# Optimization experiments

Hardware: AMD Instinct MI355X
Metric: run time of the kernel (lower is better)

Reference implementation:

```python
import jax, jax.numpy as jnp
import numpy as np

# RT-DETR multi-scale deformable attention reference (PPMSDeformableAttention forward, value_mask=None)
SPATIAL_SHAPES = ((80, 80), (40, 40), (20, 20))  # (H, W) per level; sum(H*W) = 8400 = Len_v
NUM_HEADS = 8
NUM_LEVELS = 3
NUM_POINTS = 4


def _gather_corner(v_l, ix, iy, H, W):
    # v_l: [bs, heads, H*W, hd]; ix/iy: [bs, heads, N] int32 pixel indices (possibly out of range)
    valid = (ix >= 0) & (ix < W) & (iy >= 0) & (iy < H)
    idx = jnp.clip(iy, 0, H - 1) * W + jnp.clip(ix, 0, W - 1)
    g = jnp.take_along_axis(v_l, idx[..., None], axis=2)  # [bs, heads, N, hd]
    return jnp.where(valid[..., None], g, jnp.zeros((), v_l.dtype))


def _bilinear_sample(v_l, px, py, H, W):
    # grid_sample(align_corners=False, padding_mode='zeros') semantics.
    # v_l: [bs, heads, H*W, hd]; px/py: [bs, heads, N] continuous pixel coords
    x0 = jnp.floor(px).astype(jnp.int32)
    y0 = jnp.floor(py).astype(jnp.int32)
    x1, y1 = x0 + 1, y0 + 1
    wx1 = px - x0.astype(px.dtype)
    wy1 = py - y0.astype(py.dtype)
    wx0, wy0 = 1.0 - wx1, 1.0 - wy1
    out = (_gather_corner(v_l, x0, y0, H, W) * (wx0 * wy0)[..., None]
           + _gather_corner(v_l, x1, y0, H, W) * (wx1 * wy0)[..., None]
           + _gather_corner(v_l, x0, y1, H, W) * (wx0 * wy1)[..., None]
           + _gather_corner(v_l, x1, y1, H, W) * (wx1 * wy1)[..., None])
    return out  # [bs, heads, N, hd]


def setup_inputs() -> dict:
    key = jax.random.key(0)
    ks = jax.random.split(key, 8)
    bs, Lq, C = 32, 300, 256
    Lv = sum(h * w for h, w in SPATIAL_SHAPES)
    tp = NUM_HEADS * NUM_LEVELS * NUM_POINTS  # 96
    s = 1.0 / np.sqrt(C)
    return {
        "query": jax.random.normal(ks[0], (bs, Lq, C), jnp.float32),
        "reference_points": jax.random.uniform(ks[1], (bs, Lq, NUM_LEVELS, 4), jnp.float32, 0.05, 0.95),
        "value": jax.random.normal(ks[2], (bs, Lv, C), jnp.float32),
        "Wv": jax.random.normal(ks[3], (C, C), jnp.float32) * s,
        "bv": jnp.zeros((C,), jnp.float32),
        "Woff": jax.random.normal(ks[4], (C, tp * 2), jnp.float32) * (s * 0.1),
        "boff": jax.random.normal(ks[5], (tp * 2,), jnp.float32) * 0.5,
        "Watt": jax.random.normal(ks[6], (C, tp), jnp.float32) * s,
        "batt": jnp.zeros((tp,), jnp.float32),
        "Wout": jax.random.normal(ks[7], (C, C), jnp.float32) * s,
        "bout": jnp.zeros((C,), jnp.float32),
    }


def reference(query, reference_points, value, Wv, bv, Woff, boff, Watt, batt, Wout, bout):
    bs, Lq, C = query.shape
    H_, L, P = NUM_HEADS, NUM_LEVELS, NUM_POINTS
    hd = C // H_
    Lv = value.shape[1]

    # value projection -> [bs, heads, Lv, hd]
    v = (value @ Wv + bv).reshape(bs, Lv, H_, hd).transpose(0, 2, 1, 3)

    # sampling offsets and attention weights from query
    off = (query @ Woff + boff).reshape(bs, Lq, H_, L, P, 2)
    attw = jax.nn.softmax((query @ Watt + batt).reshape(bs, Lq, H_, L * P), axis=-1)
    attw = attw.reshape(bs, Lq, H_, L, P)

    # reference_points last dim == 4: (cx, cy, w, h) normalized
    ref_xy = reference_points[:, :, None, :, None, :2]  # [bs,Lq,1,L,1,2]
    ref_wh = reference_points[:, :, None, :, None, 2:]
    loc = ref_xy + off / P * ref_wh * 0.5  # [bs,Lq,H,L,P,2], normalized [0,1]

    out = jnp.zeros((bs, Lq, H_, hd), query.dtype)
    start = 0
    for l, (H, W) in enumerate(SPATIAL_SHAPES):
        v_l = v[:, :, start:start + H * W]  # [bs, heads, H*W, hd]
        start += H * W
        # normalized -> pixel coords (align_corners=False): p = loc * size - 0.5
        locl = loc[:, :, :, l]  # [bs, Lq, heads, P, 2]
        px = locl[..., 0] * W - 0.5
        py = locl[..., 1] * H - 0.5
        # [bs, Lq, heads, P] -> [bs, heads, Lq*P]
        px = px.transpose(0, 2, 1, 3).reshape(bs, H_, Lq * P)
        py = py.transpose(0, 2, 1, 3).reshape(bs, H_, Lq * P)
        sampled = _bilinear_sample(v_l, px, py, H, W)  # [bs, heads, Lq*P, hd]
        sampled = sampled.reshape(bs, H_, Lq, P, hd)
        out = out + jnp.einsum('bhqpd,bqhp->bqhd', sampled, attw[:, :, :, l])

    out = out.reshape(bs, Lq, C)
    return out @ Wout + bout
```

## Files before the change

kernel.cpp:

```cpp
#include <hip/hip_runtime.h>
#include <hip/hip_bf16.h>

#define BS 32
#define LQ 300
#define CDIM 256
#define HEADS 8
#define HD 32
#define NLEVELS 3
#define NPOINTS 4
#define LV 8400
#define NOA 288

typedef __attribute__((ext_vector_type(4))) float f32x4;
typedef __attribute__((ext_vector_type(8))) short short8;
typedef __attribute__((ext_vector_type(8))) unsigned short u16x8;
typedef __attribute__((ext_vector_type(4))) unsigned short u16x4;

__device__ __forceinline__ unsigned short f2bf(float f) {
    __hip_bfloat16 h = __float2bfloat16(f);
    return __bfloat16_as_ushort(h);
}
__device__ __forceinline__ float bf2f(unsigned short u) {
    union { unsigned u; float f; } v; v.u = ((unsigned)u) << 16;
    return v.f;
}

__global__ void prep_weights_kernel(
    const float* __restrict__ Wv, const float* __restrict__ Wout,
    const float* __restrict__ Woff, const float* __restrict__ Watt,
    unsigned short* __restrict__ WvT, unsigned short* __restrict__ WoutT,
    unsigned short* __restrict__ WoaT)
{
    const int bid = blockIdx.x;
    const int k = threadIdx.x;
    if (bid < 256) {
        WvT[bid * 256 + k] = f2bf(Wv[k * 256 + bid]);
    } else if (bid < 512) {
        const int n = bid - 256;
        WoutT[n * 256 + k] = f2bf(Wout[k * 256 + n]);
    } else {
        const int n = bid - 512;
        const float w = (n < 192) ? Woff[k * 192 + n] : Watt[k * 96 + (n - 192)];
        WoaT[n * 256 + k] = f2bf(w);
    }
}

#define BM 128
#define BK 32
#define PAD 40
#define EP2 136
#define NT (CDIM / BK)

__global__ __launch_bounds__(256) void proj_value_mfma(
    const float* __restrict__ value, const unsigned short* __restrict__ WvT,
    const float* __restrict__ bv, unsigned short* __restrict__ vout)
{
    __shared__ alignas(16) unsigned short lds_raw[17408];
    unsigned short* lds_x = lds_raw;
    unsigned short* lds_ep = lds_raw;

    const int tid = threadIdx.x;
    const int lane = tid & 63;
    const int wave = tid >> 6;
    const int la = lane & 15;
    const int lg = lane >> 4;

    const int orig = blockIdx.x;
    const int xcd = orig & 7, lin = orig >> 3;
    const int bid = xcd * 525 + lin;
    const int n0 = (bid & 1) * 128;
    const long row0 = (long)(bid >> 1) * BM;

    const int sr = tid >> 1;
    const int sk = (tid & 1) * 16;
    const float* xptr = value + (row0 + sr) * (long)CDIM + sk;

    const unsigned short* wlane = WvT + (size_t)(n0 + wave * 32 + la) * CDIM + lg * 8;

    f32x4 xrg[4];

    auto load_tile = [&](int kb) {
        const float* p = xptr + kb;
        xrg[0] = *(const f32x4*)(p);
        xrg[1] = *(const f32x4*)(p + 4);
        xrg[2] = *(const f32x4*)(p + 8);
        xrg[3] = *(const f32x4*)(p + 12);
    };
    auto write_tile = [&](int buf) {
        u16x8 t0, t1;
#pragma unroll
        for (int i = 0; i < 4; ++i) {
            t0[i]     = f2bf(xrg[0][i]);
            t0[i + 4] = f2bf(xrg[1][i]);
            t1[i]     = f2bf(xrg[2][i]);
            t1[i + 4] = f2bf(xrg[3][i]);
        }
        u16x8* wx = (u16x8*)&lds_x[buf * (128 * PAD) + sr * PAD + sk];
        wx[0] = t0; wx[1] = t1;
    };

    f32x4 acc[2][8] = {};

    load_tile(0);
    write_tile(0);
    __syncthreads();
    int cur = 0;

#pragma unroll
    for (int t = 0; t < NT; ++t) {
        if (t + 1 < NT) load_tile((t + 1) * BK);

        short8 wf[2];
#pragma unroll
        for (int nf = 0; nf < 2; ++nf)
            wf[nf] = *(const short8*)(wlane + (size_t)nf * 16 * CDIM + t * 32);

        const unsigned short* px = &lds_x[cur * (128 * PAD) + la * PAD + lg * 8];
#pragma unroll
        for (int mf = 0; mf < 8; ++mf) {
            const short8 xf = *(const short8*)(px + mf * 16 * PAD);
#pragma unroll
            for (int nf = 0; nf < 2; ++nf)
                acc[nf][mf] = __builtin_amdgcn_mfma_f32_16x16x32_bf16(
                    wf[nf], xf, acc[nf][mf], 0, 0, 0);
        }

        if (t + 1 < NT) write_tile(cur ^ 1);
        __syncthreads();
        cur ^= 1;
    }

#pragma unroll
    for (int nf = 0; nf < 2; ++nf) {
        const int nbl = wave * 32 + nf * 16 + lg * 4;
        const f32x4 bb = *(const f32x4*)&bv[n0 + nbl];
#pragma unroll
        for (int mf = 0; mf < 8; ++mf) {
            const int mloc = mf * 16 + la;
            u16x4 o;
#pragma unroll
            for (int j = 0; j < 4; ++j) o[j] = f2bf(acc[nf][mf][j] + bb[j]);
            *(u16x4*)&lds_ep[mloc * EP2 + nbl] = o;
        }
    }
    __syncthreads();
    {
        const int er = tid >> 1;
        const int ec = (tid & 1) * 64;
        const u16x8* src = (const u16x8*)&lds_ep[er * EP2 + ec];
        u16x8* dst = (u16x8*)&vout[(row0 + er) * CDIM + n0 + ec];
#pragma unroll
        for (int i = 0; i < 8; ++i) dst[i] = src[i];
    }
}

#define APAD 40
#define BPAD 40

__global__ __launch_bounds__(256) void offatt_gemm_mfma(
    const float* __restrict__ query, const unsigned short* __restrict__ WoaT,
    const float* __restrict__ boff, const float* __restrict__ batt,
    float* __restrict__ offatt)
{
    __shared__ unsigned short lds_a[2][BM * APAD];
    __shared__ unsigned short lds_b[2][NOA * BPAD];

    const int tid = threadIdx.x;
    const int lane = tid & 63;
    const int wave = tid >> 6;
    const int wm = wave >> 1;
    const int wn = wave & 1;
    const long row0 = (long)blockIdx.x * BM;

    const int ar = tid >> 1;
    const int ak = (tid & 1) * 16;
    const float* aptr = query + (row0 + ar) * CDIM + ak;
    const unsigned short* bptr  = WoaT + (size_t)tid * CDIM;
    const unsigned short* bptr2 = WoaT + (size_t)(256 + tid) * CDIM;
    const bool extra = tid < 32;

    f32x4 arg[4];
    u16x8 brg[4], brg2[4];

    auto load_tile = [&](int kb) {
        const float* p = aptr + kb;
        arg[0] = *(const f32x4*)(p);
        arg[1] = *(const f32x4*)(p + 4);
        arg[2] = *(const f32x4*)(p + 8);
        arg[3] = *(const f32x4*)(p + 12);
        const u16x8* q = (const u16x8*)(bptr + kb);
        brg[0] = q[0]; brg[1] = q[1]; brg[2] = q[2]; brg[3] = q[3];
        if (extra) {
            const u16x8* q2 = (const u16x8*)(bptr2 + kb);
            brg2[0] = q2[0]; brg2[1] = q2[1]; brg2[2] = q2[2]; brg2[3] = q2[3];
        }
    };
    auto write_tile = [&](int buf) {
        u16x8 t0, t1;
#pragma unroll
        for (int i = 0; i < 4; ++i) {
            t0[i]     = f2bf(arg[0][i]);
            t0[i + 4] = f2bf(arg[1][i]);
            t1[i]     = f2bf(arg[2][i]);
            t1[i + 4] = f2bf(arg[3][i]);
        }
        u16x8* wa = (u16x8*)&lds_a[buf][ar * APAD + ak];
        wa[0] = t0; wa[1] = t1;
        u16x8* wb = (u16x8*)&lds_b[buf][tid * BPAD];
        wb[0] = brg[0]; wb[1] = brg[1]; wb[2] = brg[2]; wb[3] = brg[3];
        if (extra) {
            u16x8* wb2 = (u16x8*)&lds_b[buf][(256 + tid) * BPAD];
            wb2[0] = brg2[0]; wb2[1] = brg2[1]; wb2[2] = brg2[2]; wb2[3] = brg2[3];
        }
    };

    f32x4 acc[4][9] = {};
    const int la = lane & 15;
    const int lg = lane >> 4;

    load_tile(0);
    write_tile(0);
    __syncthreads();
    int cur = 0;

    for (int t = 0; t < CDIM / BK; ++t) {
        if (t + 1 < CDIM / BK) load_tile((t + 1) * BK);

        const unsigned short* pa = &lds_a[cur][(wm * 64 + la) * APAD + lg * 8];
        const unsigned short* pb = &lds_b[cur][(wn * 144 + la) * BPAD + lg * 8];
        short8 af[4];
#pragma unroll
        for (int mi = 0; mi < 4; ++mi)
            af[mi] = *(const short8*)(pa + mi * 16 * APAD);
#pragma unroll
        for (int ni = 0; ni < 9; ++ni) {
            const short8 bf = *(const short8*)(pb + ni * 16 * BPAD);
#pragma unroll
            for (int mi = 0; mi < 4; ++mi)
                acc[mi][ni] = __builtin_amdgcn_mfma_f32_16x16x32_bf16(af[mi], bf, acc[mi][ni], 0, 0, 0);
        }

        if (t + 1 < CDIM / BK) write_tile(cur ^ 1);
        __syncthreads();
        cur ^= 1;
    }

    float bias[9];
#pragma unroll
    for (int ni = 0; ni < 9; ++ni) {
        const int col = wn * 144 + ni * 16 + la;
        bias[ni] = (col < 192) ? boff[col] : batt[col - 192];
    }
#pragma unroll
    for (int mi = 0; mi < 4; ++mi) {
#pragma unroll
        for (int ni = 0; ni < 9; ++ni) {
            const int col = wn * 144 + ni * 16 + la;
#pragma unroll
            for (int j = 0; j < 4; ++j) {
                const long r = row0 + wm * 64 + mi * 16 + lg * 4 + j;
                offatt[r * NOA + col] = acc[mi][ni][j] + bias[ni];
            }
        }
    }
}

__global__ __launch_bounds__(256) void sample_kernel(
    const float* __restrict__ offatt, const float* __restrict__ refpts,
    const unsigned short* __restrict__ v, unsigned short* __restrict__ mid)
{
    __shared__ float oa_s[NOA];
    __shared__ float aw_s[96];
    __shared__ float px_s[96];
    __shared__ float py_s[96];

    const int tid = threadIdx.x;
    const int nb = blockIdx.x;
    const int x = nb & 7;
    const int rest = nb >> 3;
    const int g = rest / LQ;
    const int q = rest % LQ;
    const int b = g * 8 + x;
    const long bq = (long)b * LQ + q;

    oa_s[tid] = offatt[bq * NOA + tid];
    if (tid < 32) oa_s[256 + tid] = offatt[bq * NOA + 256 + tid];
    __syncthreads();

    if (tid < 8) {
        float m = -1e30f;
#pragma unroll
        for (int i = 0; i < 12; ++i) m = fmaxf(m, oa_s[192 + tid * 12 + i]);
        float e[12];
        float s = 0.f;
#pragma unroll
        for (int i = 0; i < 12; ++i) { e[i] = __expf(oa_s[192 + tid * 12 + i] - m); s += e[i]; }
        const float inv = 1.f / s;
#pragma unroll
        for (int i = 0; i < 12; ++i) aw_s[tid * 12 + i] = e[i] * inv;
    }
    if (tid >= 128 && tid < 224) {
        const int t = tid - 128;
        const int h = t / 12, idx = t % 12, lvl = idx >> 2, p = idx & 3;
        const float* rp = refpts + (bq * NLEVELS + lvl) * 4;
        const float rx = rp[0], ry = rp[1], rw = rp[2], rh = rp[3];
        const float ox = oa_s[((h * NLEVELS + lvl) * NPOINTS + p) * 2 + 0];
        const float oy = oa_s[((h * NLEVELS + lvl) * NPOINTS + p) * 2 + 1];
        const float lx = rx + ox * 0.125f * rw;
        const float ly = ry + oy * 0.125f * rh;
        const int Wl = 80 >> lvl;
        px_s[t] = lx * (float)Wl - 0.5f;
        py_s[t] = ly * (float)Wl - 0.5f;
    }
    __syncthreads();

    const int h = tid >> 5;
    const int pg = (tid >> 3) & 3;
    const int d4 = tid & 7;
    const unsigned short* vb = v + ((size_t)b * LV) * CDIM + h * HD + d4 * 4;

    float a0 = 0.f, a1 = 0.f, a2 = 0.f, a3 = 0.f;
#pragma unroll
    for (int j = 0; j < 3; ++j) {
        const int i = pg * 3 + j;
        const int lvl = i >> 2;
        const int idx = h * 12 + i;
        const float px = px_s[idx], py = py_s[idx], aw = aw_s[idx];
        const int Wl = 80 >> lvl;
        const int start = (lvl == 0) ? 0 : (lvl == 1) ? 6400 : 8000;

        const float fx = floorf(px), fy = floorf(py);
        const int x0 = (int)fx, y0 = (int)fy;
        const float wx1 = px - fx, wy1 = py - fy;
        const float wx0 = 1.f - wx1, wy0 = 1.f - wy1;
        const float w00 = wx0 * wy0 * aw, w10 = wx1 * wy0 * aw;
        const float w01 = wx0 * wy1 * aw, w11 = wx1 * wy1 * aw;
        const bool x0v = (unsigned)x0 < (unsigned)Wl;
        const bool x1v = (unsigned)(x0 + 1) < (unsigned)Wl;
        const bool y0v = (unsigned)y0 < (unsigned)Wl;
        const bool y1v = (unsigned)(y0 + 1) < (unsigned)Wl;

        const unsigned short* base = vb + (size_t)start * CDIM;
        if (y0v) {
            const unsigned short* r0p = base + (size_t)(y0 * Wl) * CDIM;
            if (x0v) {
                const u16x4 u = *(const u16x4*)(r0p + (size_t)x0 * CDIM);
                a0 = fmaf(w00, bf2f(u[0]), a0); a1 = fmaf(w00, bf2f(u[1]), a1);
                a2 = fmaf(w00, bf2f(u[2]), a2); a3 = fmaf(w00, bf2f(u[3]), a3);
            }
            if (x1v) {
                const u16x4 u = *(const u16x4*)(r0p + (size_t)(x0 + 1) * CDIM);
                a0 = fmaf(w10, bf2f(u[0]), a0); a1 = fmaf(w10, bf2f(u[1]), a1);
                a2 = fmaf(w10, bf2f(u[2]), a2); a3 = fmaf(w10, bf2f(u[3]), a3);
            }
        }
        if (y1v) {
            const unsigned short* r1p = base + (size_t)((y0 + 1) * Wl) * CDIM;
            if (x0v) {
                const u16x4 u = *(const u16x4*)(r1p + (size_t)x0 * CDIM);
                a0 = fmaf(w01, bf2f(u[0]), a0); a1 = fmaf(w01, bf2f(u[1]), a1);
                a2 = fmaf(w01, bf2f(u[2]), a2); a3 = fmaf(w01, bf2f(u[3]), a3);
            }
            if (x1v) {
                const u16x4 u = *(const u16x4*)(r1p + (size_t)(x0 + 1) * CDIM);
                a0 = fmaf(w11, bf2f(u[0]), a0); a1 = fmaf(w11, bf2f(u[1]), a1);
                a2 = fmaf(w11, bf2f(u[2]), a2); a3 = fmaf(w11, bf2f(u[3]), a3);
            }
        }
    }

    a0 += __shfl_xor(a0, 8);  a1 += __shfl_xor(a1, 8);
    a2 += __shfl_xor(a2, 8);  a3 += __shfl_xor(a3, 8);
    a0 += __shfl_xor(a0, 16); a1 += __shfl_xor(a1, 16);
    a2 += __shfl_xor(a2, 16); a3 += __shfl_xor(a3, 16);

    if (pg == 0) {
        u16x4 o;
        o[0] = f2bf(a0); o[1] = f2bf(a1); o[2] = f2bf(a2); o[3] = f2bf(a3);
        *(u16x4*)&mid[bq * CDIM + h * HD + d4 * 4] = o;
    }
}

__global__ __launch_bounds__(256) void out_gemm_mfma(
    const unsigned short* __restrict__ mid, const unsigned short* __restrict__ WoutT,
    const float* __restrict__ bout, float* __restrict__ out)
{
    __shared__ unsigned short lds_w[2][256 * APAD];
    __shared__ unsigned short lds_x[2][BM * BPAD];

    const int tid = threadIdx.x;
    const int lane = tid & 63;
    const int wave = tid >> 6;
    const int wn = wave & 1;
    const int wm = wave >> 1;
    const long row0 = (long)blockIdx.x * BM;

    const unsigned short* wptr = WoutT + (size_t)tid * CDIM;
    const int xr = tid >> 1;
    const int xk = (tid & 1) * 16;
    const unsigned short* xptr = mid + (row0 + xr) * CDIM + xk;

    u16x8 wrg[4];
    u16x8 xrg[2];

    auto load_tile = [&](int kb) {
        const u16x8* qw = (const u16x8*)(wptr + kb);
        wrg[0] = qw[0]; wrg[1] = qw[1]; wrg[2] = qw[2]; wrg[3] = qw[3];
        const u16x8* qx = (const u16x8*)(xptr + kb);
        xrg[0] = qx[0]; xrg[1] = qx[1];
    };
    auto write_tile = [&](int buf) {
        u16x8* ww = (u16x8*)&lds_w[buf][tid * APAD];
        ww[0] = wrg[0]; ww[1] = wrg[1]; ww[2] = wrg[2]; ww[3] = wrg[3];
        u16x8* wx = (u16x8*)&lds_x[buf][xr * BPAD + xk];
        wx[0] = xrg[0]; wx[1] = xrg[1];
    };

    f32x4 acc[8][4] = {};
    const int la = lane & 15;
    const int lg = lane >> 4;

    load_tile(0);
    write_tile(0);
    __syncthreads();
    int cur = 0;

    for (int t = 0; t < CDIM / BK; ++t) {
        if (t + 1 < CDIM / BK) load_tile((t + 1) * BK);

        const unsigned short* pw = &lds_w[cur][(wn * 128 + la) * APAD + lg * 8];
        const unsigned short* px = &lds_x[cur][(wm * 64 + la) * BPAD + lg * 8];
        short8 xf[4];
#pragma unroll
        for (int mf = 0; mf < 4; ++mf)
            xf[mf] = *(const short8*)(px + mf * 16 * BPAD);
#pragma unroll
        for (int nf = 0; nf < 8; ++nf) {
            const short8 wf = *(const short8*)(pw + nf * 16 * APAD);
#pragma unroll
            for (int mf = 0; mf < 4; ++mf)
                acc[nf][mf] = __builtin_amdgcn_mfma_f32_16x16x32_bf16(wf, xf[mf], acc[nf][mf], 0, 0, 0);
        }

        if (t + 1 < CDIM / BK) write_tile(cur ^ 1);
        __syncthreads();
        cur ^= 1;
    }

#pragma unroll
    for (int nf = 0; nf < 8; ++nf) {
        const int nbase = wn * 128 + nf * 16 + lg * 4;
        const f32x4 bb = *(const f32x4*)&bout[nbase];
#pragma unroll
        for (int mf = 0; mf < 4; ++mf) {
            const long m = row0 + wm * 64 + mf * 16 + la;
            f32x4 o;
#pragma unroll
            for (int j = 0; j < 4; ++j) o[j] = acc[nf][mf][j] + bb[j];
            *(f32x4*)&out[m * CDIM + nbase] = o;
        }
    }
}

extern "C" void kernel_launch(void* const* d_in, const int* in_sizes, int n_in,
                              void* d_out, int out_size, void* d_ws, size_t ws_size,
                              hipStream_t stream) {
    const float* query = (const float*)d_in[0];
    const float* refp  = (const float*)d_in[1];
    const float* value = (const float*)d_in[2];
    const float* Wv    = (const float*)d_in[3];
    const float* bv    = (const float*)d_in[4];
    const float* Woff  = (const float*)d_in[5];
    const float* boff  = (const float*)d_in[6];
    const float* Watt  = (const float*)d_in[7];
    const float* batt  = (const float*)d_in[8];
    const float* Wout  = (const float*)d_in[9];
    const float* bout  = (const float*)d_in[10];
    float* out = (float*)d_out;

    char* ws = (char*)d_ws;
    unsigned short* v = (unsigned short*)ws;
    size_t off = (size_t)BS * LV * CDIM * 2;
    float* offatt = (float*)(ws + off);
    off += (size_t)BS * LQ * NOA * 4;
    unsigned short* mid = (unsigned short*)(ws + off);
    off += (size_t)BS * LQ * CDIM * 2;
    unsigned short* WvT = (unsigned short*)(ws + off);
    off += 256 * 256 * 2;
    unsigned short* WoaT = (unsigned short*)(ws + off);
    off += NOA * 256 * 2;
    unsigned short* WoutT = (unsigned short*)(ws + off);

    prep_weights_kernel<<<800, 256, 0, stream>>>(Wv, Wout, Woff, Watt, WvT, WoutT, WoaT);
    proj_value_mfma<<<(BS * LV) / BM * 2, 256, 0, stream>>>(value, WvT, bv, v);
    offatt_gemm_mfma<<<(BS * LQ) / BM, 256, 0, stream>>>(query, WoaT, boff, batt, offatt);
    sample_kernel<<<BS * LQ, 256, 0, stream>>>(offatt, refp, v, mid);
    out_gemm_mfma<<<(BS * LQ) / BM, 256, 0, stream>>>(mid, WoutT, bout, out);
}
```

Measured before the change: 216.7 us.

## Compute full N per block in value projection to avoid duplicate input reads

```diff
diff --git a/kernel.cpp b/kernel.cpp
--- a/kernel.cpp
+++ b/kernel.cpp
@@ -23,6 +23,12 @@
 __device__ __forceinline__ float bf2f(unsigned short u) {
     union { unsigned u; float f; } v; v.u = ((unsigned)u) << 16;
     return v.f;
+}
+__device__ __forceinline__ u16x8 cvt8u(const f32x4 a, const f32x4 b) {
+    u16x8 c;
+#pragma unroll
+    for (int i = 0; i < 4; ++i) { c[i] = f2bf(a[i]); c[i + 4] = f2bf(b[i]); }
+    return c;
 }
 
 __global__ void prep_weights_kernel(
@@ -47,17 +53,14 @@
 
 #define BM 128
 #define BK 32
-#define PAD 40
-#define EP2 136
+#define XPAD 264
 #define NT (CDIM / BK)
 
 __global__ __launch_bounds__(256) void proj_value_mfma(
     const float* __restrict__ value, const unsigned short* __restrict__ WvT,
     const float* __restrict__ bv, unsigned short* __restrict__ vout)
 {
-    __shared__ alignas(16) unsigned short lds_raw[17408];
-    unsigned short* lds_x = lds_raw;
-    unsigned short* lds_ep = lds_raw;
+    __shared__ alignas(16) unsigned short lds_x[128 * XPAD];
 
     const int tid = threadIdx.x;
     const int lane = tid & 63;
@@ -67,90 +70,64 @@
 
     const int orig = blockIdx.x;
     const int xcd = orig & 7, lin = orig >> 3;
-    const int bid = xcd * 525 + lin;
-    const int n0 = (bid & 1) * 128;
-    const long row0 = (long)(bid >> 1) * BM;
-
-    const int sr = tid >> 1;
-    const int sk = (tid & 1) * 16;
-    const float* xptr = value + (row0 + sr) * (long)CDIM + sk;
-
-    const unsigned short* wlane = WvT + (size_t)(n0 + wave * 32 + la) * CDIM + lg * 8;
-
-    f32x4 xrg[4];
-
-    auto load_tile = [&](int kb) {
-        const float* p = xptr + kb;
-        xrg[0] = *(const f32x4*)(p);
-        xrg[1] = *(const f32x4*)(p + 4);
-        xrg[2] = *(const f32x4*)(p + 8);
-        xrg[3] = *(const f32x4*)(p + 12);
-    };
-    auto write_tile = [&](int buf) {
-        u16x8 t0, t1;
-#pragma unroll
-        for (int i = 0; i < 4; ++i) {
-            t0[i]     = f2bf(xrg[0][i]);
-            t0[i + 4] = f2bf(xrg[1][i]);
-            t1[i]     = f2bf(xrg[2][i]);
-            t1[i + 4] = f2bf(xrg[3][i]);
-        }
-        u16x8* wx = (u16x8*)&lds_x[buf * (128 * PAD) + sr * PAD + sk];
-        wx[0] = t0; wx[1] = t1;
-    };
-
-    f32x4 acc[2][8] = {};
-
-    load_tile(0);
-    write_tile(0);
-    __syncthreads();
-    int cur = 0;
+    const int bid = (xcd < 4 ? xcd * 263 : 4 * 263 + (xcd - 4) * 262) + lin;
+    const long row0 = (long)bid * BM;
+
+#pragma unroll
+    for (int i = 0; i < 16; ++i) {
+        const int p = i * 256 + tid;
+        const int row = p >> 5;
+        const int c8 = (p & 31) * 8;
+        const float* src = value + (row0 + row) * (long)CDIM + c8;
+        const f32x4 a = *(const f32x4*)(src);
+        const f32x4 b = *(const f32x4*)(src + 4);
+        *(u16x8*)&lds_x[row * XPAD + c8] = cvt8u(a, b);
+    }
+    __syncthreads();
+
+    const unsigned short* wlane = WvT + (size_t)(wave * 64 + la) * CDIM + lg * 8;
+
+    f32x4 acc[4][8] = {};
 
 #pragma unroll
     for (int t = 0; t < NT; ++t) {
-        if (t + 1 < NT) load_tile((t + 1) * BK);
-
-        short8 wf[2];
-#pragma unroll
-        for (int nf = 0; nf < 2; ++nf)
+        short8 wf[4];
+#pragma unroll
+        for (int nf = 0; nf < 4; ++nf)
             wf[nf] = *(const short8*)(wlane + (size_t)nf * 16 * CDIM + t * 32);
-
-        const unsigned short* px = &lds_x[cur * (128 * PAD) + la * PAD + lg * 8];
+        const unsigned short* px = &lds_x[la * XPAD + t * 32 + lg * 8];
 #pragma unroll
         for (int mf = 0; mf < 8; ++mf) {
-            const short8 xf = *(const short8*)(px + mf * 16 * PAD);
-#pragma unroll
-            for (int nf = 0; nf < 2; ++nf)
+            const short8 xf = *(const short8*)(px + mf * 16 * XPAD);
+#pragma unroll
+            for (int nf = 0; nf < 4; ++nf)
                 acc[nf][mf] = __builtin_amdgcn_mfma_f32_16x16x32_bf16(
                     wf[nf], xf, acc[nf][mf], 0, 0, 0);
         }
-
-        if (t + 1 < NT) write_tile(cur ^ 1);
-        __syncthreads();
-        cur ^= 1;
-    }
-
-#pragma unroll
-    for (int nf = 0; nf < 2; ++nf) {
-        const int nbl = wave * 32 + nf * 16 + lg * 4;
-        const f32x4 bb = *(const f32x4*)&bv[n0 + nbl];
+    }
+
+    __syncthreads();
+#pragma unroll
+    for (int nf = 0; nf < 4; ++nf) {
+        const int nbl = wave * 64 + nf * 16 + lg * 4;
+        const f32x4 bb = *(const f32x4*)&bv[nbl];
 #pragma unroll
         for (int mf = 0; mf < 8; ++mf) {
             const int mloc = mf * 16 + la;
             u16x4 o;
 #pragma unroll
             for (int j = 0; j < 4; ++j) o[j] = f2bf(acc[nf][mf][j] + bb[j]);
-            *(u16x4*)&lds_ep[mloc * EP2 + nbl] = o;
+            *(u16x4*)&lds_x[mloc * XPAD + nbl] = o;
         }
     }
     __syncthreads();
     {
         const int er = tid >> 1;
-        const int ec = (tid & 1) * 64;
-        const u16x8* src = (const u16x8*)&lds_ep[er * EP2 + ec];
-        u16x8* dst = (u16x8*)&vout[(row0 + er) * CDIM + n0 + ec];
-#pragma unroll
-        for (int i = 0; i < 8; ++i) dst[i] = src[i];
+        const int ec = (tid & 1) * 128;
+        const u16x8* src = (const u16x8*)&lds_x[er * XPAD + ec];
+        u16x8* dst = (u16x8*)&vout[(row0 + er) * CDIM + ec];
+#pragma unroll
+        for (int i = 0; i < 16; ++i) dst[i] = src[i];
     }
 }
 
@@ -492,7 +469,7 @@
     unsigned short* WoutT = (unsigned short*)(ws + off);
 
     prep_weights_kernel<<<800, 256, 0, stream>>>(Wv, Wout, Woff, Watt, WvT, WoutT, WoaT);
-    proj_value_mfma<<<(BS * LV) / BM * 2, 256, 0, stream>>>(value, WvT, bv, v);
+    proj_value_mfma<<<(BS * LV) / BM, 256, 0, stream>>>(value, WvT, bv, v);
     offatt_gemm_mfma<<<(BS * LQ) / BM, 256, 0, stream>>>(query, WoaT, boff, batt, offatt);
     sample_kernel<<<BS * LQ, 256, 0, stream>>>(offatt, refp, v, mid);
     out_gemm_mfma<<<(BS * LQ) / BM, 256, 0, stream>>>(mid, WoutT, bout, out);
```

Measured after the change: 282.2 us. 30.2% more time.

## Retile value projection to full-width 128x256 blocks staging Wv in LDS

Applied to the files above, without the earlier changes.

```diff
diff --git a/kernel.cpp b/kernel.cpp
--- a/kernel.cpp
+++ b/kernel.cpp
@@ -46,47 +46,53 @@
 }
 
 #define BM 128
-#define BK 32
-#define PAD 40
-#define EP2 136
-#define NT (CDIM / BK)
-
-__global__ __launch_bounds__(256) void proj_value_mfma(
+#define BKP 64
+#define PADP 72
+#define EPAD 264
+#define NTP (CDIM / BKP)
+
+__global__ __launch_bounds__(512) void proj_value_mfma(
     const float* __restrict__ value, const unsigned short* __restrict__ WvT,
     const float* __restrict__ bv, unsigned short* __restrict__ vout)
 {
-    __shared__ alignas(16) unsigned short lds_raw[17408];
-    unsigned short* lds_x = lds_raw;
+    __shared__ alignas(16) unsigned short lds_raw[27648];
+    unsigned short* lds_w = lds_raw;
+    unsigned short* lds_x = lds_raw + 256 * PADP;
     unsigned short* lds_ep = lds_raw;
 
     const int tid = threadIdx.x;
     const int lane = tid & 63;
     const int wave = tid >> 6;
+    const int wm = wave >> 2;
+    const int wn = wave & 3;
     const int la = lane & 15;
     const int lg = lane >> 4;
 
     const int orig = blockIdx.x;
     const int xcd = orig & 7, lin = orig >> 3;
-    const int bid = xcd * 525 + lin;
-    const int n0 = (bid & 1) * 128;
-    const long row0 = (long)(bid >> 1) * BM;
-
-    const int sr = tid >> 1;
-    const int sk = (tid & 1) * 16;
-    const float* xptr = value + (row0 + sr) * (long)CDIM + sk;
-
-    const unsigned short* wlane = WvT + (size_t)(n0 + wave * 32 + la) * CDIM + lg * 8;
-
+    const int bid = (xcd < 4 ? xcd * 263 : 4 * 263 + (xcd - 4) * 262) + lin;
+    const long row0 = (long)bid * BM;
+
+    const int wr = tid >> 1, wk = (tid & 1) * 32;
+    const unsigned short* wptr = WvT + (size_t)wr * CDIM + wk;
+    const int xr = tid >> 2, xk = (tid & 3) * 16;
+    const float* xptr = value + (row0 + xr) * (long)CDIM + xk;
+
+    u16x8 wrg[4];
     f32x4 xrg[4];
 
     auto load_tile = [&](int kb) {
+        const u16x8* qw = (const u16x8*)(wptr + kb);
+        wrg[0] = qw[0]; wrg[1] = qw[1]; wrg[2] = qw[2]; wrg[3] = qw[3];
         const float* p = xptr + kb;
         xrg[0] = *(const f32x4*)(p);
         xrg[1] = *(const f32x4*)(p + 4);
         xrg[2] = *(const f32x4*)(p + 8);
         xrg[3] = *(const f32x4*)(p + 12);
     };
-    auto write_tile = [&](int buf) {
+    auto write_tile = [&]() {
+        u16x8* ww = (u16x8*)&lds_w[wr * PADP + wk];
+        ww[0] = wrg[0]; ww[1] = wrg[1]; ww[2] = wrg[2]; ww[3] = wrg[3];
         u16x8 t0, t1;
 #pragma unroll
         for (int i = 0; i < 4; ++i) {
@@ -95,65 +101,71 @@
             t1[i]     = f2bf(xrg[2][i]);
             t1[i + 4] = f2bf(xrg[3][i]);
         }
-        u16x8* wx = (u16x8*)&lds_x[buf * (128 * PAD) + sr * PAD + sk];
+        u16x8* wx = (u16x8*)&lds_x[xr * PADP + xk];
         wx[0] = t0; wx[1] = t1;
     };
 
-    f32x4 acc[2][8] = {};
+    f32x4 acc[4][4] = {};
 
     load_tile(0);
-    write_tile(0);
-    __syncthreads();
-    int cur = 0;
-
-#pragma unroll
-    for (int t = 0; t < NT; ++t) {
-        if (t + 1 < NT) load_tile((t + 1) * BK);
-
-        short8 wf[2];
-#pragma unroll
-        for (int nf = 0; nf < 2; ++nf)
-            wf[nf] = *(const short8*)(wlane + (size_t)nf * 16 * CDIM + t * 32);
-
-        const unsigned short* px = &lds_x[cur * (128 * PAD) + la * PAD + lg * 8];
-#pragma unroll
-        for (int mf = 0; mf < 8; ++mf) {
-            const short8 xf = *(const short8*)(px + mf * 16 * PAD);
-#pragma unroll
-            for (int nf = 0; nf < 2; ++nf)
-                acc[nf][mf] = __builtin_amdgcn_mfma_f32_16x16x32_bf16(
-                    wf[nf], xf, acc[nf][mf], 0, 0, 0);
-        }
-
-        if (t + 1 < NT) write_tile(cur ^ 1);
+
+#pragma unroll
+    for (int t = 0; t < NTP; ++t) {
         __syncthreads();
-        cur ^= 1;
-    }
-
-#pragma unroll
-    for (int nf = 0; nf < 2; ++nf) {
-        const int nbl = wave * 32 + nf * 16 + lg * 4;
-        const f32x4 bb = *(const f32x4*)&bv[n0 + nbl];
-#pragma unroll
-        for (int mf = 0; mf < 8; ++mf) {
-            const int mloc = mf * 16 + la;
-            u16x4 o;
-#pragma unroll
-            for (int j = 0; j < 4; ++j) o[j] = f2bf(acc[nf][mf][j] + bb[j]);
-            *(u16x4*)&lds_ep[mloc * EP2 + nbl] = o;
-        }
-    }
-    __syncthreads();
-    {
-        const int er = tid >> 1;
-        const int ec = (tid & 1) * 64;
-        const u16x8* src = (const u16x8*)&lds_ep[er * EP2 + ec];
-        u16x8* dst = (u16x8*)&vout[(row0 + er) * CDIM + n0 + ec];
-#pragma unroll
-        for (int i = 0; i < 8; ++i) dst[i] = src[i];
-    }
-}
-
+        write_tile();
+        __syncthreads();
+        if (t + 1 < NTP) load_tile((t + 1) * BKP);
+
+#pragma unroll
+        for (int kk = 0; kk < 2; ++kk) {
+            const unsigned short* pw = &lds_w[(wn * 64 + la) * PADP + kk * 32 + lg * 8];
+            const unsigned short* px = &lds_x[(wm * 64 + la) * PADP + kk * 32 + lg * 8];
+            short8 xf[4];
+#pragma unroll
+            for (int mf = 0; mf < 4; ++mf)
+                xf[mf] = *(const short8*)(px + mf * 16 * PADP);
+#pragma unroll
+            for (int nf = 0; nf < 4; ++nf) {
+                const short8 wf = *(const short8*)(pw + nf * 16 * PADP);
+#pragma unroll
+                for (int mf = 0; mf < 4; ++mf)
+                    acc[nf][mf] = __builtin_amdgcn_mfma_f32_16x16x32_bf16(
+                        wf, xf[mf], acc[nf][mf], 0, 0, 0);
+            }
+        }
+    }
+
+#pragma unroll
+    for (int pass = 0; pass < 2; ++pass) {
+        __syncthreads();
+        if (wm == pass) {
+#pragma unroll
+            for (int nf = 0; nf < 4; ++nf) {
+                const int nbl = wn * 64 + nf * 16 + lg * 4;
+                const f32x4 bb = *(const f32x4*)&bv[nbl];
+#pragma unroll
+                for (int mf = 0; mf < 4; ++mf) {
+                    const int mloc = mf * 16 + la;
+                    u16x4 o;
+#pragma unroll
+                    for (int j = 0; j < 4; ++j) o[j] = f2bf(acc[nf][mf][j] + bb[j]);
+                    *(u16x4*)&lds_ep[mloc * EPAD + nbl] = o;
+                }
+            }
+        }
+        __syncthreads();
+        const int er = tid >> 3;
+        const int ec = (tid & 7) * 32;
+        const long gr = row0 + pass * 64 + er;
+        const u16x8* src = (const u16x8*)&lds_ep[er * EPAD + ec];
+        u16x8* dst = (u16x8*)&vout[gr * CDIM + ec];
+#pragma unroll
+        for (int i = 0; i < 4; ++i) dst[i] = src[i];
+    }
+}
+
+#define BMQ 128
+#define BKQ 32
 #define APAD 40
 #define BPAD 40
 
@@ -162,7 +174,7 @@
     const float* __restrict__ boff, const float* __restrict__ batt,
     float* __restrict__ offatt)
 {
-    __shared__ unsigned short lds_a[2][BM * APAD];
+    __shared__ unsigned short lds_a[2][BMQ * APAD];
     __shared__ unsigned short lds_b[2][NOA * BPAD];
 
     const int tid = threadIdx.x;
@@ -170,7 +182,7 @@
     const int wave = tid >> 6;
     const int wm = wave >> 1;
     const int wn = wave & 1;
-    const long row0 = (long)blockIdx.x * BM;
+    const long row0 = (long)blockIdx.x * BMQ;
 
     const int ar = tid >> 1;
     const int ak = (tid & 1) * 16;
@@ -223,8 +235,8 @@
     __syncthreads();
     int cur = 0;
 
-    for (int t = 0; t < CDIM / BK; ++t) {
-        if (t + 1 < CDIM / BK) load_tile((t + 1) * BK);
+    for (int t = 0; t < CDIM / BKQ; ++t) {
+        if (t + 1 < CDIM / BKQ) load_tile((t + 1) * BKQ);
 
         const unsigned short* pa = &lds_a[cur][(wm * 64 + la) * APAD + lg * 8];
         const unsigned short* pb = &lds_b[cur][(wn * 144 + la) * BPAD + lg * 8];
@@ -240,7 +252,7 @@
                 acc[mi][ni] = __builtin_amdgcn_mfma_f32_16x16x32_bf16(af[mi], bf, acc[mi][ni], 0, 0, 0);
         }
 
-        if (t + 1 < CDIM / BK) write_tile(cur ^ 1);
+        if (t + 1 < CDIM / BKQ) write_tile(cur ^ 1);
         __syncthreads();
         cur ^= 1;
     }
@@ -386,14 +398,14 @@
     const float* __restrict__ bout, float* __restrict__ out)
 {
     __shared__ unsigned short lds_w[2][256 * APAD];
-    __shared__ unsigned short lds_x[2][BM * BPAD];
+    __shared__ unsigned short lds_x[2][BMQ * BPAD];
 
     const int tid = threadIdx.x;
     const int lane = tid & 63;
     const int wave = tid >> 6;
     const int wn = wave & 1;
     const int wm = wave >> 1;
-    const long row0 = (long)blockIdx.x * BM;
+    const long row0 = (long)blockIdx.x * BMQ;
 
     const unsigned short* wptr = WoutT + (size_t)tid * CDIM;
     const int xr = tid >> 1;
@@ -425,8 +437,8 @@
     __syncthreads();
     int cur = 0;
 
-    for (int t = 0; t < CDIM / BK; ++t) {
-        if (t + 1 < CDIM / BK) load_tile((t + 1) * BK);
+    for (int t = 0; t < CDIM / BKQ; ++t) {
+        if (t + 1 < CDIM / BKQ) load_tile((t + 1) * BKQ);
 
         const unsigned short* pw = &lds_w[cur][(wn * 128 + la) * APAD + lg * 8];
         const unsigned short* px = &lds_x[cur][(wm * 64 + la) * BPAD + lg * 8];
@@ -442,7 +454,7 @@
                 acc[nf][mf] = __builtin_amdgcn_mfma_f32_16x16x32_bf16(wf, xf[mf], acc[nf][mf], 0, 0, 0);
         }
 
-        if (t + 1 < CDIM / BK) write_tile(cur ^ 1);
+        if (t + 1 < CDIM / BKQ) write_tile(cur ^ 1);
         __syncthreads();
         cur ^= 1;
     }
@@ -492,8 +504,8 @@
     unsigned short* WoutT = (unsigned short*)(ws + off);
 
     prep_weights_kernel<<<800, 256, 0, stream>>>(Wv, Wout, Woff, Watt, WvT, WoutT, WoaT);
-    proj_value_mfma<<<(BS * LV) / BM * 2, 256, 0, stream>>>(value, WvT, bv, v);
-    offatt_gemm_mfma<<<(BS * LQ) / BM, 256, 0, stream>>>(query, WoaT, boff, batt, offatt);
+    proj_value_mfma<<<(BS * LV) / BM, 512, 0, stream>>>(value, WvT, bv, v);
+    offatt_gemm_mfma<<<(BS * LQ) / BMQ, 256, 0, stream>>>(query, WoaT, boff, batt, offatt);
     sample_kernel<<<BS * LQ, 256, 0, stream>>>(offatt, refp, v, mid);
-    out_gemm_mfma<<<(BS * LQ) / BM, 256, 0, stream>>>(mid, WoutT, bout, out);
-}
+    out_gemm_mfma<<<(BS * LQ) / BMQ, 256, 0, stream>>>(mid, WoutT, bout, out);
+}
```

Result: faster. 205.0 us (-5.4%).
